# Kernel tuning notes

Measured on AMD Instinct MI355X. Metric: run time of the kernel, lower is better.

Reference implementation:

```python
import jax, jax.numpy as jnp
import numpy as np

N, E, C = 100000, 3200000, 30
IN, HID, OUT = 256, 256, 64


def _shapley_tables(max_n):
    # Closed form of the ShapleyGNNLayer per-node contribution:
    #   deg n == 0           : contrib = 0
    #   1 <= n <= 5 (exact)  : contrib = a(n)*x_i + b(n)*T_i,  a(n)=H_{n+1}/(n+1),
    #                          b(n) = -(H_{n+1}-1)/(n(n+1))   (H = harmonic number)
    #   n > 5 (Monte Carlo)  : permutation sum telescopes -> contrib = T_i/n exactly
    # where T_i = sum of neighbor features.
    H = np.concatenate([[0.0], np.cumsum(1.0 / np.arange(1, max_n + 2))])
    a = np.zeros(max_n + 1)
    b = np.zeros(max_n + 1)
    for m in range(1, max_n + 1):
        if m <= 5:
            a[m] = H[m + 1] / (m + 1)
            b[m] = -(H[m + 1] - 1.0) / (m * (m + 1))
        else:
            b[m] = 1.0 / m
    return jnp.asarray(a, jnp.float32), jnp.asarray(b, jnp.float32)


def _shapley_layer(x, mask, n_deg, a_tab, b_tab, W):
    T = mask @ x                                # [C,D] sum of neighbor feats
    a = a_tab[n_deg][:, None]
    b = b_tab[n_deg][:, None]
    sh = x + a * x + b * T                      # shapley_matrix (x[i] + contrib)
    return jax.nn.relu(sh @ W)


def setup_inputs() -> dict:
    key = jax.random.key(0)
    ks = jax.random.split(key, 10)
    s = 0.05
    return {
        "x": jax.random.normal(ks[0], (N, IN), jnp.float32),
        "edge_index": jax.random.randint(ks[1], (2, E), 0, N, dtype=jnp.int64)
        if jax.config.jax_enable_x64 else jax.random.randint(ks[1], (2, E), 0, N),
        "W_assign": jax.random.normal(ks[2], (IN, C), jnp.float32) * s,
        "b_assign": jnp.zeros((C,), jnp.float32),
        "W_proj": jax.random.normal(ks[3], (IN, IN), jnp.float32) * s,
        "b_proj": jnp.zeros((IN,), jnp.float32),
        "W_sh1": jax.random.normal(ks[4], (IN, HID), jnp.float32) * s,
        "W_sh2": jax.random.normal(ks[5], (HID, HID), jnp.float32) * s,
        "W_out": jax.random.normal(ks[6], (HID, OUT), jnp.float32) * s,
        "b_out": jnp.zeros((OUT,), jnp.float32),
    }


def reference(x, edge_index, W_assign, b_assign, W_proj, b_proj, W_sh1, W_sh2, W_out, b_out):
    n_nodes = x.shape[0]
    row, col = edge_index[0], edge_index[1]

    # --- MinCutPoolLayerSparse ---
    S = jax.nn.softmax(x @ W_assign + b_assign, axis=-1)        # [N,C]
    X_proj = x @ W_proj + b_proj                                 # [N,IN]
    Z = S.T @ X_proj                                             # [C,IN]
    adj_S = jax.ops.segment_sum(S[col], row, num_segments=n_nodes)   # A @ S, [N,C]
    adj_new = S.T @ adj_S                                        # [C,C]
    deg = jax.ops.segment_sum(jnp.ones((row.shape[0],), x.dtype), row,
                              num_segments=n_nodes)              # [N]
    vol = jnp.sum(S * deg[:, None])                              # trace(S^T D)
    cut = jnp.trace(adj_new)
    mincut_loss = -cut / (vol + 1e-9)
    SS = S.T @ S
    ortho_loss = jnp.linalg.norm(SS - jnp.eye(S.shape[1], dtype=S.dtype))

    # --- pooled edge structure (adj_pooled > 0) ---
    mask = (adj_new > 0).astype(x.dtype)                         # [C,C]
    n_deg = jnp.sum(adj_new > 0, axis=1)                         # [C] int
    a_tab, b_tab = _shapley_tables(S.shape[1])

    # --- Shapley GNN layers ---
    h = _shapley_layer(Z, mask, n_deg, a_tab, b_tab, W_sh1)
    h = _shapley_layer(h, mask, n_deg, a_tab, b_tab, W_sh2)
    out = h @ W_out + b_out
    return (out, mincut_loss, ortho_loss, Z, S)
```

## Files before the change

### kernel.cpp

```cpp
#include <hip/hip_runtime.h>
#include <math.h>

typedef float f32x4 __attribute__((ext_vector_type(4)));

#define N_NODES 100000
#define C_CL 30
#define D_IN 256

#define OUT_MAT 0
#define OUT_MC 1920
#define OUT_OR 1921
#define OUT_Z 1922
#define OUT_S 9602

#define WS_M 0
#define WS_SS 7680
#define WS_CS 8580
#define WS_CUT 8610
#define WS_H1 8640
#define WS_S8 32256
#define WS_SLAB0 1771008

#define SLAB_SS2 7680
#define SLAB_CS2 8580
#define SLAB_STRIDE2 8640
#define MAX_R 512

#define CHUNK 128
#define NCHUNK ((N_NODES + CHUNK - 1) / CHUNK)

__global__ __launch_bounds__(256, 4)
void k_node(const float* __restrict__ x, const float* __restrict__ Wa,
            const float* __restrict__ ba, float* __restrict__ S_out,
            unsigned* __restrict__ S8) {
  __shared__ float lg[64][33];
  __shared__ float lwf[8192];
  const int t = threadIdx.x;
  const int lane = t & 63;
  const int cg = __builtin_amdgcn_readfirstlane(t >> 6);

  #pragma unroll 8
  for (int it = 0; it < 32; ++it) {
    const int idx = it * 256 + t;
    const int k = 4 * (idx >> 7) + (idx & 3);
    const int c = (idx >> 2) & 31;
    lwf[idx] = (c < C_CL) ? Wa[k * C_CL + c] : 0.f;
  }

  const int node = blockIdx.x * 64 + lane;
  const bool valid = (node < N_NODES);
  const int node_c = valid ? node : (N_NODES - 1);
  const f32x4* __restrict__ xr =
      reinterpret_cast<const f32x4*>(x) + (size_t)node_c * 64;
  const float4* __restrict__ lw4 = reinterpret_cast<const float4*>(lwf);
  __syncthreads();

  float acc[8];
  #pragma unroll
  for (int j = 0; j < 8; ++j) acc[j] = 0.f;

  #pragma unroll 8
  for (int k4 = 0; k4 < 64; ++k4) {
    const f32x4 xv = xr[k4];
    #pragma unroll
    for (int j = 0; j < 8; ++j) {
      const float4 wv = lw4[k4 * 32 + cg * 8 + j];
      acc[j] += xv.x * wv.x + xv.y * wv.y + xv.z * wv.z + xv.w * wv.w;
    }
  }
  #pragma unroll
  for (int j = 0; j < 8; ++j) lg[lane][cg * 8 + j] = acc[j];
  __syncthreads();

  if (t < 64) {
    if (valid) {
      float v[C_CL];
      float mx = -3.0e38f;
      #pragma unroll
      for (int c = 0; c < C_CL; ++c) {
        v[c] = lg[t][c] + ba[c];
        mx = fmaxf(mx, v[c]);
      }
      float sm = 0.f;
      #pragma unroll
      for (int c = 0; c < C_CL; ++c) { v[c] = __expf(v[c] - mx); sm += v[c]; }
      const float r = 1.f / sm;
      #pragma unroll
      for (int c = 0; c < C_CL; ++c) lg[t][c] = v[c] * r;
    } else {
      #pragma unroll
      for (int c = 0; c < C_CL; ++c) lg[t][c] = 0.f;
    }
    lg[t][30] = 0.f; lg[t][31] = 0.f;
  }
  __syncthreads();

  const int gbase = blockIdx.x * 1920;
  #pragma unroll
  for (int i = 0; i < 8; ++i) {
    const unsigned idx = i * 256 + t;
    if (idx < 1920u) {
      const unsigned n = idx / 30u, c = idx - 30u * n;
      const int g = gbase + (int)idx;
      if (g < N_NODES * C_CL) S_out[g] = lg[n][c];
    }
  }
  const unsigned sbase = (unsigned)blockIdx.x * 512;
  #pragma unroll
  for (int i = 0; i < 2; ++i) {
    const unsigned idx = i * 256 + t;
    const unsigned n = idx >> 3, j = idx & 7;
    const unsigned b0 = (unsigned)(lg[n][j * 4 + 0] * 255.f + 0.5f);
    const unsigned b1 = (unsigned)(lg[n][j * 4 + 1] * 255.f + 0.5f);
    const unsigned b2 = (unsigned)(lg[n][j * 4 + 2] * 255.f + 0.5f);
    const unsigned b3 = (unsigned)(lg[n][j * 4 + 3] * 255.f + 0.5f);
    S8[sbase + idx] = b0 | (b1 << 8) | (b2 << 16) | (b3 << 24);
  }
}

__global__ __launch_bounds__(256, 2)
void k_M2(const float* __restrict__ x, const float* __restrict__ Sp,
          float* __restrict__ slabs, const int R) {
  __shared__ float sraw[8192];
  float (*sm)[32] = reinterpret_cast<float (*)[32]>(sraw);
  const int t = threadIdx.x;
  const int h = t >> 7, sub = (t >> 6) & 1, lc = t & 63;
  const int i4 = (t >> 3) & 7, j4 = t & 7, w = t >> 6;
  const f32x4* __restrict__ x4 = reinterpret_cast<const f32x4*>(x);

  float a[16][4];
  #pragma unroll
  for (int j = 0; j < 16; ++j) { a[j][0] = 0.f; a[j][1] = 0.f; a[j][2] = 0.f; a[j][3] = 0.f; }
  float ssq[16];
  #pragma unroll
  for (int j = 0; j < 16; ++j) ssq[j] = 0.f;
  float cs = 0.f;

  for (int chunk = blockIdx.x; chunk < NCHUNK; chunk += R) {
    const int node0 = chunk * CHUNK;
    const int rows_valid = N_NODES - node0;
    __syncthreads();
    #pragma unroll
    for (int i = 0; i < 15; ++i) {
      const int idx = i * 256 + t;
      const int n = idx / 30, c = idx - 30 * n;
      const int g = node0 * C_CL + idx;
      sm[n][c] = (g < N_NODES * C_CL) ? Sp[g] : 0.f;
    }
    sm[t & 127][30 + (t >> 7)] = 0.f;
    __syncthreads();

    if (rows_valid >= CHUNK) {
      #pragma unroll 4
      for (int n = 0; n < 64; ++n) {
        const int nn = sub * 64 + n;
        const f32x4 xv = __builtin_nontemporal_load(&x4[(size_t)(node0 + nn) * 64 + lc]);
        const float4 s0 = *reinterpret_cast<const float4*>(&sm[nn][h * 16 + 0]);
        const float4 s1 = *reinterpret_cast<const float4*>(&sm[nn][h * 16 + 4]);
        const float4 s2 = *reinterpret_cast<const float4*>(&sm[nn][h * 16 + 8]);
        const float4 s3 = *reinterpret_cast<const float4*>(&sm[nn][h * 16 + 12]);
        const float sv[16] = {s0.x, s0.y, s0.z, s0.w, s1.x, s1.y, s1.z, s1.w,
                              s2.x, s2.y, s2.z, s2.w, s3.x, s3.y, s3.z, s3.w};
        #pragma unroll
        for (int j = 0; j < 16; ++j) {
          a[j][0] += sv[j] * xv.x; a[j][1] += sv[j] * xv.y;
          a[j][2] += sv[j] * xv.z; a[j][3] += sv[j] * xv.w;
        }
      }
    } else {
      for (int n = 0; n < 64; ++n) {
        const int nn = sub * 64 + n;
        f32x4 xv = (f32x4)0.f;
        if (nn < rows_valid) xv = x4[(size_t)(node0 + nn) * 64 + lc];
        const float4 s0 = *reinterpret_cast<const float4*>(&sm[nn][h * 16 + 0]);
        const float4 s1 = *reinterpret_cast<const float4*>(&sm[nn][h * 16 + 4]);
        const float4 s2 = *reinterpret_cast<const float4*>(&sm[nn][h * 16 + 8]);
        const float4 s3 = *reinterpret_cast<const float4*>(&sm[nn][h * 16 + 12]);
        const float sv[16] = {s0.x, s0.y, s0.z, s0.w, s1.x, s1.y, s1.z, s1.w,
                              s2.x, s2.y, s2.z, s2.w, s3.x, s3.y, s3.z, s3.w};
        #pragma unroll
        for (int j = 0; j < 16; ++j) {
          a[j][0] += sv[j] * xv.x; a[j][1] += sv[j] * xv.y;
          a[j][2] += sv[j] * xv.z; a[j][3] += sv[j] * xv.w;
        }
      }
    }

    #pragma unroll 4
    for (int n = 0; n < 32; ++n) {
      const int nn = w * 32 + n;
      const float4 av = *reinterpret_cast<const float4*>(&sm[nn][i4 * 4]);
      const float4 bv = *reinterpret_cast<const float4*>(&sm[nn][j4 * 4]);
      const float af[4] = {av.x, av.y, av.z, av.w};
      const float bf[4] = {bv.x, bv.y, bv.z, bv.w};
      #pragma unroll
      for (int ii = 0; ii < 4; ++ii)
        #pragma unroll
        for (int jj = 0; jj < 4; ++jj) ssq[ii * 4 + jj] += af[ii] * bf[jj];
    }
    if (t < C_CL) {
      #pragma unroll 4
      for (int n = 0; n < CHUNK; ++n) cs += sm[n][t];
    }
  }

  float* __restrict__ slab = slabs + (size_t)blockIdx.x * SLAB_STRIDE2;
  __syncthreads();
  if (sub == 1) {
    #pragma unroll
    for (int j = 0; j < 16; ++j) {
      const int c = h * 16 + j;
      if (c < C_CL) {
        #pragma unroll
        for (int q = 0; q < 4; ++q) sraw[c * 256 + lc * 4 + q] = a[j][q];
      }
    }
  }
  __syncthreads();
  if (sub == 0) {
    #pragma unroll
    for (int j = 0; j < 16; ++j) {
      const int c = h * 16 + j;
      if (c < C_CL) {
        #pragma unroll
        for (int q = 0; q < 4; ++q)
          slab[c * 256 + lc * 4 + q] = a[j][q] + sraw[c * 256 + lc * 4 + q];
      }
    }
  }
  __syncthreads();
  #pragma unroll
  for (int ii = 0; ii < 4; ++ii) {
    #pragma unroll
    for (int jj = 0; jj < 4; ++jj) {
      const int gi = i4 * 4 + ii, gj = j4 * 4 + jj;
      if (gi < C_CL && gj < C_CL)
        sraw[w * 900 + gi * C_CL + gj] = ssq[ii * 4 + jj];
    }
  }
  __syncthreads();
  for (int q = t; q < 900; q += 256)
    slab[SLAB_SS2 + q] = (sraw[q] + sraw[900 + q]) + (sraw[1800 + q] + sraw[2700 + q]);
  if (t < C_CL) slab[SLAB_CS2 + t] = cs;
}

__global__ __launch_bounds__(256)
void k_reduce(const float* __restrict__ slabs, const int R,
              float* __restrict__ ws) {
  const int i = blockIdx.x * 256 + threadIdx.x;
  if (i == 0) ws[WS_CUT] = 0.f;
  if (i >= 8610) return;
  float s = 0.f;
  int r = 0;
  for (; r + 16 <= R; r += 16) {
    const float* p = slabs + (size_t)r * SLAB_STRIDE2 + i;
    float v[16];
    #pragma unroll
    for (int q = 0; q < 16; ++q) v[q] = p[(size_t)q * SLAB_STRIDE2];
    float s0 = ((v[0] + v[1]) + (v[2] + v[3])) + ((v[4] + v[5]) + (v[6] + v[7]));
    float s1 = ((v[8] + v[9]) + (v[10] + v[11])) + ((v[12] + v[13]) + (v[14] + v[15]));
    s += s0 + s1;
  }
  for (; r < R; ++r) s += slabs[(size_t)r * SLAB_STRIDE2 + i];
  ws[i] = s;
}

__device__ __forceinline__ int dd(unsigned a, unsigned b, int acc) {
  acc += (int)((a & 0xffu) * (b & 0xffu));
  acc += (int)(((a >> 8) & 0xffu) * ((b >> 8) & 0xffu));
  acc += (int)(((a >> 16) & 0xffu) * ((b >> 16) & 0xffu));
  acc += (int)((a >> 24) * (b >> 24));
  return acc;
}

__global__ __launch_bounds__(256)
void k_edges(const int* __restrict__ ei, const int E,
             const unsigned* __restrict__ S8, float* __restrict__ ws) {
  const int t = threadIdx.x;
  const int tid = blockIdx.x * 256 + t;
  const int* __restrict__ row = ei;
  const int* __restrict__ col = ei + E;
  float acc = 0.f;
  for (int e = tid; e < E; e += gridDim.x * 256) {
    const int r = row[e], c = col[e];
    const uint4* pr = reinterpret_cast<const uint4*>(S8 + (size_t)r * 8);
    const uint4* pc = reinterpret_cast<const uint4*>(S8 + (size_t)c * 8);
    const uint4 a0 = pr[0], a1 = pr[1];
    const uint4 b0 = pc[0], b1 = pc[1];
    int s = 0;
    s = dd(a0.x, b0.x, s); s = dd(a0.y, b0.y, s);
    s = dd(a0.z, b0.z, s); s = dd(a0.w, b0.w, s);
    s = dd(a1.x, b1.x, s); s = dd(a1.y, b1.y, s);
    s = dd(a1.z, b1.z, s); s = dd(a1.w, b1.w, s);
    acc += (float)s;
  }
  acc *= (1.f / 65025.f);
  #pragma unroll
  for (int m = 1; m < 64; m <<= 1) acc += __shfl_xor(acc, m, 64);
  __shared__ float wsum[4];
  if ((t & 63) == 0) wsum[t >> 6] = acc;
  __syncthreads();
  if (t == 0)
    atomicAdd(&ws[WS_CUT], wsum[0] + wsum[1] + wsum[2] + wsum[3]);
}

__global__ __launch_bounds__(256)
void k_z1(const float* __restrict__ ws, const float* __restrict__ Wp,
          const float* __restrict__ bp, const float* __restrict__ W1,
          float* __restrict__ out, float* __restrict__ h1out) {
  __shared__ float Mr[256], Mc[256], sh[256];
  const int r = blockIdx.x, t = threadIdx.x;
  float mc = 0.f;
  #pragma unroll
  for (int rr = 0; rr < C_CL; ++rr) mc += ws[WS_M + rr * 256 + t];
  Mc[t] = mc;
  Mr[t] = ws[WS_M + r * 256 + t];
  float scs = 0.f;
  #pragma unroll
  for (int rr = 0; rr < C_CL; ++rr) scs += ws[WS_CS + rr];
  __syncthreads();
  const float bpt = bp[t];
  float az = ws[WS_CS + r] * bpt;
  float ac = scs * bpt;
  #pragma unroll 8
  for (int k = 0; k < 256; ++k) {
    const float wv = Wp[(size_t)k * 256 + t];
    az += Mr[k] * wv;
    ac += Mc[k] * wv;
  }
  out[OUT_Z + r * 256 + t] = az;
  sh[t] = az + (1.f / 30.f) * ac;
  __syncthreads();
  float a1 = 0.f;
  #pragma unroll 8
  for (int k = 0; k < 256; ++k) a1 += sh[k] * W1[(size_t)k * 256 + t];
  h1out[r * 256 + t] = fmaxf(a1, 0.f);
}

__global__ __launch_bounds__(256)
void k_z2(const float* __restrict__ ws, const float* __restrict__ W2,
          const float* __restrict__ Wo, const float* __restrict__ bo,
          float* __restrict__ out, const float vol) {
  __shared__ float sh[256];
  __shared__ float h2[256];
  __shared__ float red[4][64];
  __shared__ float wsum[4];
  const int r = blockIdx.x, t = threadIdx.x;
  if (r < C_CL) {
    float cs1 = 0.f;
    #pragma unroll
    for (int rr = 0; rr < C_CL; ++rr) cs1 += ws[WS_H1 + rr * 256 + t];
    sh[t] = ws[WS_H1 + r * 256 + t] + (1.f / 30.f) * cs1;
    __syncthreads();
    float a2 = 0.f;
    #pragma unroll 8
    for (int k = 0; k < 256; ++k) a2 += sh[k] * W2[(size_t)k * 256 + t];
    h2[t] = fmaxf(a2, 0.f);
    __syncthreads();
    const int c = t & 63, q = t >> 6;
    float ao = 0.f;
    #pragma unroll 8
    for (int k = q * 64; k < q * 64 + 64; ++k) ao += h2[k] * Wo[k * 64 + c];
    red[q][c] = ao;
    __syncthreads();
    if (t < 64)
      out[OUT_MAT + r * 64 + t] =
          bo[t] + ((red[0][t] + red[1][t]) + (red[2][t] + red[3][t]));
  } else {
    float s = 0.f;
    for (int i = t; i < 900; i += 256) {
      const float d = ws[WS_SS + i] - ((i / C_CL == i % C_CL) ? 1.f : 0.f);
      s += d * d;
    }
    #pragma unroll
    for (int m = 1; m < 64; m <<= 1) s += __shfl_xor(s, m, 64);
    if ((t & 63) == 0) wsum[t >> 6] = s;
    __syncthreads();
    if (t == 0) {
      out[OUT_OR] = sqrtf(wsum[0] + wsum[1] + wsum[2] + wsum[3]);
      out[OUT_MC] = -ws[WS_CUT] / (vol + 1e-9f);
    }
  }
}

extern "C" void kernel_launch(void* const* d_in, const int* in_sizes, int n_in,
                              void* d_out, int out_size, void* d_ws, size_t ws_size,
                              hipStream_t stream) {
  (void)n_in; (void)out_size;
  const float* x  = (const float*)d_in[0];
  const int*   ei = (const int*)d_in[1];
  const float* Wa = (const float*)d_in[2];
  const float* ba = (const float*)d_in[3];
  const float* Wp = (const float*)d_in[4];
  const float* bp = (const float*)d_in[5];
  const float* W1 = (const float*)d_in[6];
  const float* W2 = (const float*)d_in[7];
  const float* Wo = (const float*)d_in[8];
  const float* bo = (const float*)d_in[9];
  float* out = (float*)d_out;
  float* ws  = (float*)d_ws;
  unsigned* S8 = (unsigned*)(ws + WS_S8);
  float* slabs = ws + WS_SLAB0;
  const int E = in_sizes[1] / 2;

  long avail = (long)(ws_size / 4) - WS_SLAB0;
  int R = (int)(avail / SLAB_STRIDE2);
  if (R > MAX_R) R = MAX_R;
  if (R < 1) R = 1;

  k_node<<<1563, 256, 0, stream>>>(x, Wa, ba, out + OUT_S, S8);
  k_M2<<<R, 256, 0, stream>>>(x, out + OUT_S, slabs, R);
  k_reduce<<<34, 256, 0, stream>>>(slabs, R, ws);
  k_edges<<<4096, 256, 0, stream>>>(ei, E, S8, ws);
  k_z1<<<C_CL, 256, 0, stream>>>(ws, Wp, bp, W1, out, ws + WS_H1);
  k_z2<<<C_CL + 1, 256, 0, stream>>>(ws, W2, Wo, bo, out, (float)E);
}
```

Measured before the change: 468.0 us.

## Fuse M2 reduction and edge cut pass into one kernel with atomics

Merges the per-block slab accumulation, the separate slab reduction kernel and the edge cut kernel into a single kernel. Partial sums now go straight into the workspace through atomicAdd, and a new prep kernel zeroes those accumulators. The prep kernel also pre-transposes W_assign into the float4 layout, so k_node reads it from global memory instead of staging it in LDS on every block. This removes two launches and the slab write and readback traffic, at the cost of atomic contention on about 8.6K addresses, nondeterministic float summation order, and W reads that now go through cache instead of LDS.

Result: faster. 435.6 us (-6.9%).

```diff
diff --git a/kernel.cpp b/kernel.cpp
--- a/kernel.cpp
+++ b/kernel.cpp
@@ -18,42 +18,47 @@
 #define WS_CS 8580
 #define WS_CUT 8610
 #define WS_H1 8640
+#define WS_WT4 24000
 #define WS_S8 32256
-#define WS_SLAB0 1771008
-
-#define SLAB_SS2 7680
-#define SLAB_CS2 8580
-#define SLAB_STRIDE2 8640
-#define MAX_R 512
+
+#define GRID_M2 512
 
 #define CHUNK 128
 #define NCHUNK ((N_NODES + CHUNK - 1) / CHUNK)
 
+__global__ __launch_bounds__(256)
+void k_prep(const float* __restrict__ Wa, float* __restrict__ ws) {
+  const int b = blockIdx.x, t = threadIdx.x;
+  if (b < 8) {
+    const int g = b * 256 + t;
+    const int k4 = g >> 5, c = g & 31;
+    float4 v = make_float4(0.f, 0.f, 0.f, 0.f);
+    if (c < C_CL) {
+      v.x = Wa[(4 * k4 + 0) * C_CL + c];
+      v.y = Wa[(4 * k4 + 1) * C_CL + c];
+      v.z = Wa[(4 * k4 + 2) * C_CL + c];
+      v.w = Wa[(4 * k4 + 3) * C_CL + c];
+    }
+    reinterpret_cast<float4*>(ws + WS_WT4)[g] = v;
+  } else {
+    for (int i = t; i < 8640; i += 256) ws[i] = 0.f;
+  }
+}
+
 __global__ __launch_bounds__(256, 4)
-void k_node(const float* __restrict__ x, const float* __restrict__ Wa,
+void k_node(const float* __restrict__ x, const float* __restrict__ wt4f,
             const float* __restrict__ ba, float* __restrict__ S_out,
             unsigned* __restrict__ S8) {
   __shared__ float lg[64][33];
-  __shared__ float lwf[8192];
   const int t = threadIdx.x;
   const int lane = t & 63;
   const int cg = __builtin_amdgcn_readfirstlane(t >> 6);
-
-  #pragma unroll 8
-  for (int it = 0; it < 32; ++it) {
-    const int idx = it * 256 + t;
-    const int k = 4 * (idx >> 7) + (idx & 3);
-    const int c = (idx >> 2) & 31;
-    lwf[idx] = (c < C_CL) ? Wa[k * C_CL + c] : 0.f;
-  }
-
   const int node = blockIdx.x * 64 + lane;
   const bool valid = (node < N_NODES);
   const int node_c = valid ? node : (N_NODES - 1);
   const f32x4* __restrict__ xr =
       reinterpret_cast<const f32x4*>(x) + (size_t)node_c * 64;
-  const float4* __restrict__ lw4 = reinterpret_cast<const float4*>(lwf);
-  __syncthreads();
+  const float4* __restrict__ wt4 = reinterpret_cast<const float4*>(wt4f);
 
   float acc[8];
   #pragma unroll
@@ -64,7 +69,7 @@
     const f32x4 xv = xr[k4];
     #pragma unroll
     for (int j = 0; j < 8; ++j) {
-      const float4 wv = lw4[k4 * 32 + cg * 8 + j];
+      const float4 wv = wt4[k4 * 32 + cg * 8 + j];
       acc[j] += xv.x * wv.x + xv.y * wv.y + xv.z * wv.z + xv.w * wv.w;
     }
   }
@@ -118,9 +123,18 @@
   }
 }
 
+__device__ __forceinline__ int dd(unsigned a, unsigned b, int acc) {
+  acc += (int)((a & 0xffu) * (b & 0xffu));
+  acc += (int)(((a >> 8) & 0xffu) * ((b >> 8) & 0xffu));
+  acc += (int)(((a >> 16) & 0xffu) * ((b >> 16) & 0xffu));
+  acc += (int)((a >> 24) * (b >> 24));
+  return acc;
+}
+
 __global__ __launch_bounds__(256, 2)
-void k_M2(const float* __restrict__ x, const float* __restrict__ Sp,
-          float* __restrict__ slabs, const int R) {
+void k_M2E(const float* __restrict__ x, const float* __restrict__ Sp,
+           float* __restrict__ ws, const int* __restrict__ ei, const int E,
+           const unsigned* __restrict__ S8) {
   __shared__ float sraw[8192];
   float (*sm)[32] = reinterpret_cast<float (*)[32]>(sraw);
   const int t = threadIdx.x;
@@ -136,7 +150,7 @@
   for (int j = 0; j < 16; ++j) ssq[j] = 0.f;
   float cs = 0.f;
 
-  for (int chunk = blockIdx.x; chunk < NCHUNK; chunk += R) {
+  for (int chunk = blockIdx.x; chunk < NCHUNK; chunk += GRID_M2) {
     const int node0 = chunk * CHUNK;
     const int rows_valid = N_NODES - node0;
     __syncthreads();
@@ -204,7 +218,6 @@
     }
   }
 
-  float* __restrict__ slab = slabs + (size_t)blockIdx.x * SLAB_STRIDE2;
   __syncthreads();
   if (sub == 1) {
     #pragma unroll
@@ -224,7 +237,8 @@
       if (c < C_CL) {
         #pragma unroll
         for (int q = 0; q < 4; ++q)
-          slab[c * 256 + lc * 4 + q] = a[j][q] + sraw[c * 256 + lc * 4 + q];
+          atomicAdd(&ws[WS_M + c * 256 + lc * 4 + q],
+                    a[j][q] + sraw[c * 256 + lc * 4 + q]);
       }
     }
   }
@@ -240,48 +254,14 @@
   }
   __syncthreads();
   for (int q = t; q < 900; q += 256)
-    slab[SLAB_SS2 + q] = (sraw[q] + sraw[900 + q]) + (sraw[1800 + q] + sraw[2700 + q]);
-  if (t < C_CL) slab[SLAB_CS2 + t] = cs;
-}
-
-__global__ __launch_bounds__(256)
-void k_reduce(const float* __restrict__ slabs, const int R,
-              float* __restrict__ ws) {
-  const int i = blockIdx.x * 256 + threadIdx.x;
-  if (i == 0) ws[WS_CUT] = 0.f;
-  if (i >= 8610) return;
-  float s = 0.f;
-  int r = 0;
-  for (; r + 16 <= R; r += 16) {
-    const float* p = slabs + (size_t)r * SLAB_STRIDE2 + i;
-    float v[16];
-    #pragma unroll
-    for (int q = 0; q < 16; ++q) v[q] = p[(size_t)q * SLAB_STRIDE2];
-    float s0 = ((v[0] + v[1]) + (v[2] + v[3])) + ((v[4] + v[5]) + (v[6] + v[7]));
-    float s1 = ((v[8] + v[9]) + (v[10] + v[11])) + ((v[12] + v[13]) + (v[14] + v[15]));
-    s += s0 + s1;
-  }
-  for (; r < R; ++r) s += slabs[(size_t)r * SLAB_STRIDE2 + i];
-  ws[i] = s;
-}
-
-__device__ __forceinline__ int dd(unsigned a, unsigned b, int acc) {
-  acc += (int)((a & 0xffu) * (b & 0xffu));
-  acc += (int)(((a >> 8) & 0xffu) * ((b >> 8) & 0xffu));
-  acc += (int)(((a >> 16) & 0xffu) * ((b >> 16) & 0xffu));
-  acc += (int)((a >> 24) * (b >> 24));
-  return acc;
-}
-
-__global__ __launch_bounds__(256)
-void k_edges(const int* __restrict__ ei, const int E,
-             const unsigned* __restrict__ S8, float* __restrict__ ws) {
-  const int t = threadIdx.x;
-  const int tid = blockIdx.x * 256 + t;
+    atomicAdd(&ws[WS_SS + q],
+              (sraw[q] + sraw[900 + q]) + (sraw[1800 + q] + sraw[2700 + q]));
+  if (t < C_CL) atomicAdd(&ws[WS_CS + t], cs);
+
   const int* __restrict__ row = ei;
   const int* __restrict__ col = ei + E;
   float acc = 0.f;
-  for (int e = tid; e < E; e += gridDim.x * 256) {
+  for (int e = blockIdx.x * 256 + t; e < E; e += GRID_M2 * 256) {
     const int r = row[e], c = col[e];
     const uint4* pr = reinterpret_cast<const uint4*>(S8 + (size_t)r * 8);
     const uint4* pc = reinterpret_cast<const uint4*>(S8 + (size_t)c * 8);
@@ -297,11 +277,11 @@
   acc *= (1.f / 65025.f);
   #pragma unroll
   for (int m = 1; m < 64; m <<= 1) acc += __shfl_xor(acc, m, 64);
-  __shared__ float wsum[4];
-  if ((t & 63) == 0) wsum[t >> 6] = acc;
+  __syncthreads();
+  if ((t & 63) == 0) sraw[t >> 6] = acc;
   __syncthreads();
   if (t == 0)
-    atomicAdd(&ws[WS_CUT], wsum[0] + wsum[1] + wsum[2] + wsum[3]);
+    atomicAdd(&ws[WS_CUT], (sraw[0] + sraw[1]) + (sraw[2] + sraw[3]));
 }
 
 __global__ __launch_bounds__(256)
@@ -386,7 +366,7 @@
 extern "C" void kernel_launch(void* const* d_in, const int* in_sizes, int n_in,
                               void* d_out, int out_size, void* d_ws, size_t ws_size,
                               hipStream_t stream) {
-  (void)n_in; (void)out_size;
+  (void)n_in; (void)out_size; (void)ws_size;
   const float* x  = (const float*)d_in[0];
   const int*   ei = (const int*)d_in[1];
   const float* Wa = (const float*)d_in[2];
@@ -400,18 +380,11 @@
   float* out = (float*)d_out;
   float* ws  = (float*)d_ws;
   unsigned* S8 = (unsigned*)(ws + WS_S8);
-  float* slabs = ws + WS_SLAB0;
   const int E = in_sizes[1] / 2;
 
-  long avail = (long)(ws_size / 4) - WS_SLAB0;
-  int R = (int)(avail / SLAB_STRIDE2);
-  if (R > MAX_R) R = MAX_R;
-  if (R < 1) R = 1;
-
-  k_node<<<1563, 256, 0, stream>>>(x, Wa, ba, out + OUT_S, S8);
-  k_M2<<<R, 256, 0, stream>>>(x, out + OUT_S, slabs, R);
-  k_reduce<<<34, 256, 0, stream>>>(slabs, R, ws);
-  k_edges<<<4096, 256, 0, stream>>>(ei, E, S8, ws);
+  k_prep<<<9, 256, 0, stream>>>(Wa, ws);
+  k_node<<<1563, 256, 0, stream>>>(x, ws + WS_WT4, ba, out + OUT_S, S8);
+  k_M2E<<<GRID_M2, 256, 0, stream>>>(x, out + OUT_S, ws, ei, E, S8);
   k_z1<<<C_CL, 256, 0, stream>>>(ws, Wp, bp, W1, out, ws + WS_H1);
   k_z2<<<C_CL + 1, 256, 0, stream>>>(ws, W2, Wo, bo, out, (float)E);
 }
```
